# Kernel optimization log

Measured on AMD Instinct MI355X. Metric: run time of the kernel, lower is better.

## Reference

```python
import jax, jax.numpy as jnp
import numpy as np

B, T, I, H = 32768, 200, 6, 6
FF, OUT = 128, 12


def setup_inputs() -> dict:
    key = jax.random.key(0)
    ks = jax.random.split(key, 10)
    s = lambda fan_in: 1.0 / np.sqrt(fan_in)
    inp = {
        "x": jax.random.normal(ks[0], (B, T, I), dtype=jnp.float32),
        # PyTorch LSTM params (gate order i, f, g, o)
        "W_ih": jax.random.uniform(ks[1], (4 * H, I), jnp.float32, -s(H), s(H)),
        "W_hh": jax.random.uniform(ks[2], (4 * H, H), jnp.float32, -s(H), s(H)),
        "b_ih": jax.random.uniform(ks[3], (4 * H,), jnp.float32, -s(H), s(H)),
        "b_hh": jax.random.uniform(ks[4], (4 * H,), jnp.float32, -s(H), s(H)),
        # MLP head (Dropout is identity in eval mode)
        "W1": jax.random.uniform(ks[5], (FF, T * H), jnp.float32, -s(T * H), s(T * H)),
        "b1": jax.random.uniform(ks[6], (FF,), jnp.float32, -s(T * H), s(T * H)),
        "W2": jax.random.uniform(ks[7], (OUT, FF), jnp.float32, -s(FF), s(FF)),
        "b2": jax.random.uniform(ks[8], (OUT,), jnp.float32, -s(FF), s(FF)),
    }
    return inp


def _lstm(x, W_ih, W_hh, b_ih, b_hh):
    # x: [B, T, I] -> hidden sequence [B, T, H]
    # Precompute input projections for all timesteps at once: [T, B, 4H]
    xg = jnp.einsum("bti,gi->tbg", x, W_ih) + (b_ih + b_hh)
    h0 = jnp.zeros((x.shape[0], H), x.dtype)
    c0 = jnp.zeros((x.shape[0], H), x.dtype)

    def step(carry, xg_t):
        h, c = carry
        gates = xg_t + h @ W_hh.T  # [B, 4H]
        i, f, g, o = jnp.split(gates, 4, axis=-1)
        i = jax.nn.sigmoid(i)
        f = jax.nn.sigmoid(f)
        g = jnp.tanh(g)
        o = jax.nn.sigmoid(o)
        c = f * c + i * g
        h = o * jnp.tanh(c)
        return (h, c), h

    _, hs = jax.lax.scan(step, (h0, c0), xg)  # hs: [T, B, H]
    return jnp.transpose(hs, (1, 0, 2))  # [B, T, H]


def reference(x, W_ih, W_hh, b_ih, b_hh, W1, b1, W2, b2):
    hs = _lstm(x, W_ih, W_hh, b_ih, b_hh)          # [B, T, H]
    flat = hs.reshape(hs.shape[0], -1)             # [B, T*H]
    hid = jax.nn.relu(flat @ W1.T + b1)            # [B, 128]
    return hid @ W2.T + b2                         # [B, 12]
```

## Files before the change

### kernel.cpp

```cpp
#include <hip/hip_runtime.h>
#include <hip/hip_bf16.h>

#define Bn   32768
#define Tn   200
#define In   6
#define Hn   6
#define FFn  128
#define OUTn 12
#define KP   1600

typedef __attribute__((ext_vector_type(2))) float          f32x2;
typedef __attribute__((ext_vector_type(4))) float          f32x4;
typedef __attribute__((ext_vector_type(8))) short          bf16x8;
typedef __attribute__((ext_vector_type(4))) unsigned short u16x4;
typedef __attribute__((ext_vector_type(8))) unsigned short u16x8;

#define LOG2E 1.442695041f

__device__ __forceinline__ f32x2 pkfma(f32x2 a, f32x2 b, f32x2 c) {
#if __has_builtin(__builtin_elementwise_fma)
    return __builtin_elementwise_fma(a, b, c);
#else
    return a * b + c;
#endif
}
__device__ __forceinline__ float rcp1p(float e) {
    return __builtin_amdgcn_rcpf(1.f + __builtin_amdgcn_exp2f(e));
}
__device__ __forceinline__ float tanh_c(float c) {
    return fmaf(-2.f, rcp1p(2.f * LOG2E * c), 1.f);
}
__device__ __forceinline__ float swap1(float v) {
    return __int_as_float(__builtin_amdgcn_mov_dpp(__float_as_int(v), 0xB1, 0xF, 0xF, true));
}
__device__ __forceinline__ unsigned short f2bf(float v) {
    unsigned u = __float_as_uint(v);
    unsigned r = u + 0x7FFFu + ((u >> 16) & 1u);
    return (unsigned short)(r >> 16);
}

#define BAR() do {                                          \
    asm volatile("s_waitcnt lgkmcnt(0)" ::: "memory");      \
    __builtin_amdgcn_sched_barrier(0);                      \
    __builtin_amdgcn_s_barrier();                           \
    __builtin_amdgcn_sched_barrier(0);                      \
} while (0)

__global__ void prep_kernel(const float* __restrict__ W1, unsigned short* __restrict__ W1p) {
    int idx = blockIdx.x * 256 + threadIdx.x;
    if (idx >= FFn * KP) return;
    int ff = idx / KP, kp = idx - ff * KP;
    int t = kp >> 3, p = kp & 7;
    float v = 0.f;
    if (p != 3 && p != 7) {
        int h = (p < 3) ? p : (p - 1);
        v = W1[ff * (Tn * Hn) + t * Hn + h];
    }
    W1p[idx] = f2bf(v);
}

__global__ __launch_bounds__(256, 1)
void fused_kernel(const float* __restrict__ x,
                  const float* __restrict__ W_ih, const float* __restrict__ W_hh,
                  const float* __restrict__ b_ih, const float* __restrict__ b_hh,
                  const unsigned short* __restrict__ W1p,
                  const float* __restrict__ b1,
                  const float* __restrict__ W2, const float* __restrict__ b2,
                  float* __restrict__ out)
{
    __shared__ unsigned short htile[2][8][128][8];
    __shared__ unsigned short hidS[128][136];
    __shared__ float          W2s[OUTn * FFn];

    const int tid  = threadIdx.x;
    const int sloc = tid >> 1;
    const int role = tid & 1;
    const int b0   = blockIdx.x * 128;
    const int wv   = tid >> 6;
    const int l    = tid & 63;
    const int lr   = l & 15;
    const int lg   = l >> 4;

    f32x2 Wx[6][6], Wh[6][6], bias2[6];
    #pragma unroll
    for (int gt = 0; gt < 4; ++gt) {
        #pragma unroll
        for (int m = 0; m < 3; ++m) {
            const int j = gt * 3 + m;
            const int p = j >> 1, hf = j & 1;
            const int row = gt * 6 + role * 3 + m;
            const float sc = (gt == 2) ? (2.f * LOG2E) : (-LOG2E);
            #pragma unroll
            for (int k = 0; k < 6; ++k) Wx[p][k][hf] = sc * W_ih[row * 6 + k];
            #pragma unroll
            for (int k = 0; k < 3; ++k) Wh[p][k][hf]     = sc * W_hh[row * 6 + role * 3 + k];
            #pragma unroll
            for (int k = 0; k < 3; ++k) Wh[p][3 + k][hf] = sc * W_hh[row * 6 + (1 - role) * 3 + k];
            bias2[p][hf] = sc * (b_ih[row] + b_hh[row]);
        }
    }

    float hOwn[3] = {0.f, 0.f, 0.f}, hOth[3] = {0.f, 0.f, 0.f}, cS[3] = {0.f, 0.f, 0.f};

    f32x4 acc[8][2];
    #pragma unroll
    for (int m = 0; m < 8; ++m)
        #pragma unroll
        for (int n = 0; n < 2; ++n)
            acc[m][n] = (f32x4){0.f, 0.f, 0.f, 0.f};

    const f32x4* xb4 = (const f32x4*)(x + (size_t)(b0 + sloc) * (Tn * In));

    const unsigned short* wrow[2];
    #pragma unroll
    for (int n = 0; n < 2; ++n) wrow[n] = W1p + (size_t)(wv * 32 + n * 16 + lr) * KP;

    auto LOADB = [&](int g, bf16x8 (&bf)[2][2]) {
        #pragma unroll
        for (int kc = 0; kc < 2; ++kc)
            #pragma unroll
            for (int n = 0; n < 2; ++n)
                bf[kc][n] = *((const bf16x8*)&wrow[n][g * 64 + kc * 32 + lg * 8]);
    };

    auto STEPS8 = [&](const f32x4 (&bx)[12], int slot) {
        #pragma unroll
        for (int s = 0; s < 8; ++s) {
            float xv[6];
            #pragma unroll
            for (int k = 0; k < 6; ++k) { const int fl = s * 6 + k; xv[k] = bx[fl >> 2][fl & 3]; }
            f32x2 a2[6];
            #pragma unroll
            for (int p = 0; p < 6; ++p) a2[p] = bias2[p];
            #pragma unroll
            for (int k = 0; k < 6; ++k) {
                const f32x2 xs = (f32x2){xv[k], xv[k]};
                #pragma unroll
                for (int p = 0; p < 6; ++p) a2[p] = pkfma(Wx[p][k], xs, a2[p]);
            }
            #pragma unroll
            for (int k = 0; k < 3; ++k) {
                const f32x2 hs = (f32x2){hOwn[k], hOwn[k]};
                #pragma unroll
                for (int p = 0; p < 6; ++p) a2[p] = pkfma(Wh[p][k], hs, a2[p]);
            }
            #pragma unroll
            for (int k = 0; k < 3; ++k) {
                const f32x2 hs = (f32x2){hOth[k], hOth[k]};
                #pragma unroll
                for (int p = 0; p < 6; ++p) a2[p] = pkfma(Wh[p][3 + k], hs, a2[p]);
            }
            float av[12];
            #pragma unroll
            for (int p = 0; p < 6; ++p) { av[2 * p] = a2[p][0]; av[2 * p + 1] = a2[p][1]; }

            unsigned short hb[3];
            #pragma unroll
            for (int m = 0; m < 3; ++m) {
                const float iv = rcp1p(av[m]);
                const float fv = rcp1p(av[3 + m]);
                const float gv = fmaf(-2.f, rcp1p(av[6 + m]), 1.f);
                const float ov = rcp1p(av[9 + m]);
                const float c  = fmaf(fv, cS[m], iv * gv);
                cS[m] = c;
                const float hv = ov * tanh_c(c);
                hOwn[m] = hv;
                hOth[m] = swap1(hv);
                hb[m]   = f2bf(hv);
            }
            u16x4 hw; hw.x = hb[0]; hw.y = hb[1]; hw.z = hb[2]; hw.w = 0;
            *((u16x4*)&htile[slot][s][sloc][role * 4]) = hw;
        }
    };

    auto MFMAG8 = [&](int slot, const bf16x8 (&bf)[2][2]) {
        #pragma unroll
        for (int kc = 0; kc < 2; ++kc) {
            bf16x8 af[8];
            #pragma unroll
            for (int m = 0; m < 8; ++m)
                af[m] = *((const bf16x8*)&htile[slot][kc * 4 + lg][m * 16 + lr][0]);
            #pragma unroll
            for (int n = 0; n < 2; ++n)
                #pragma unroll
                for (int m = 0; m < 8; ++m)
                    acc[m][n] = __builtin_amdgcn_mfma_f32_16x16x32_bf16(af[m], bf[kc][n], acc[m][n], 0, 0, 0);
        }
    };

    f32x4 bufA[12], bufB[12];
    #pragma unroll
    for (int q = 0; q < 12; ++q) bufA[q] = xb4[q];
    bf16x8 bfA[2][2], bfB[2][2];

    for (int gg = 0; gg < 12; ++gg) {
        const int gA = 2 * gg, gB = gA + 1;
        #pragma unroll
        for (int q = 0; q < 12; ++q) bufB[q] = xb4[gB * 12 + q];
        LOADB(gA, bfA);
        STEPS8(bufA, 0);
        BAR();
        #pragma unroll
        for (int q = 0; q < 12; ++q) bufA[q] = xb4[(gB + 1) * 12 + q];
        MFMAG8(0, bfA);
        LOADB(gB, bfB);
        STEPS8(bufB, 1);
        BAR();
        MFMAG8(1, bfB);
    }
    LOADB(24, bfA);
    STEPS8(bufA, 0);
    BAR();
    MFMAG8(0, bfA);

    float b1v[2];
    #pragma unroll
    for (int n = 0; n < 2; ++n) b1v[n] = b1[wv * 32 + n * 16 + lr];
    #pragma unroll
    for (int m = 0; m < 8; ++m)
        #pragma unroll
        for (int n = 0; n < 2; ++n)
            #pragma unroll
            for (int r = 0; r < 4; ++r)
                hidS[m * 16 + lg * 4 + r][wv * 32 + n * 16 + lr] =
                    f2bf(fmaxf(acc[m][n][r] + b1v[n], 0.f));
    for (int q = tid; q < OUTn * FFn; q += 256) W2s[q] = W2[q];
    __syncthreads();

    const int s2 = tid >> 1;
    const int half = tid & 1;
    float oa[6];
    #pragma unroll
    for (int jj = 0; jj < 6; ++jj) oa[jj] = b2[half * 6 + jj];
    for (int k8 = 0; k8 < 16; ++k8) {
        const u16x8 hv8 = *((const u16x8*)&hidS[s2][k8 * 8]);
        #pragma unroll
        for (int e = 0; e < 8; ++e) {
            const float hv = __uint_as_float(((unsigned)(unsigned short)hv8[e]) << 16);
            const int k = k8 * 8 + e;
            #pragma unroll
            for (int jj = 0; jj < 6; ++jj)
                oa[jj] = fmaf(hv, W2s[(half * 6 + jj) * FFn + k], oa[jj]);
        }
    }
    float* op = out + (size_t)(b0 + s2) * OUTn + half * 6;
    #pragma unroll
    for (int jj = 0; jj < 6; ++jj) op[jj] = oa[jj];
}

extern "C" void kernel_launch(void* const* d_in, const int* in_sizes, int n_in,
                              void* d_out, int out_size, void* d_ws, size_t ws_size,
                              hipStream_t stream) {
    const float* x    = (const float*)d_in[0];
    const float* W_ih = (const float*)d_in[1];
    const float* W_hh = (const float*)d_in[2];
    const float* b_ih = (const float*)d_in[3];
    const float* b_hh = (const float*)d_in[4];
    const float* W1   = (const float*)d_in[5];
    const float* b1   = (const float*)d_in[6];
    const float* W2   = (const float*)d_in[7];
    const float* b2   = (const float*)d_in[8];
    unsigned short* W1p = (unsigned short*)d_ws;
    float* out = (float*)d_out;

    prep_kernel<<<(FFn * KP + 255) / 256, 256, 0, stream>>>(W1, W1p);
    fused_kernel<<<Bn / 128, 256, 0, stream>>>(x, W_ih, W_hh, b_ih, b_hh,
                                               W1p, b1, W2, b2, out);
}
```

Baseline: 116.4 us.

## Merge LSTM gate reciprocals and restructure x prefetch into half-group buffers

```diff
diff --git a/kernel.cpp b/kernel.cpp
--- a/kernel.cpp
+++ b/kernel.cpp
@@ -23,12 +23,6 @@
 #else
     return a * b + c;
 #endif
-}
-__device__ __forceinline__ float rcp1p(float e) {
-    return __builtin_amdgcn_rcpf(1.f + __builtin_amdgcn_exp2f(e));
-}
-__device__ __forceinline__ float tanh_c(float c) {
-    return fmaf(-2.f, rcp1p(2.f * LOG2E * c), 1.f);
 }
 __device__ __forceinline__ float swap1(float v) {
     return __int_as_float(__builtin_amdgcn_mov_dpp(__float_as_int(v), 0xB1, 0xF, 0xF, true));
@@ -123,9 +117,9 @@
                 bf[kc][n] = *((const bf16x8*)&wrow[n][g * 64 + kc * 32 + lg * 8]);
     };
 
-    auto STEPS8 = [&](const f32x4 (&bx)[12], int slot) {
-        #pragma unroll
-        for (int s = 0; s < 8; ++s) {
+    auto STEPS4 = [&](const f32x4 (&bx)[6], int slot, int sbase) {
+        #pragma unroll
+        for (int s = 0; s < 4; ++s) {
             float xv[6];
             #pragma unroll
             for (int k = 0; k < 6; ++k) { const int fl = s * 6 + k; xv[k] = bx[fl >> 2][fl & 3]; }
@@ -157,19 +151,25 @@
             unsigned short hb[3];
             #pragma unroll
             for (int m = 0; m < 3; ++m) {
-                const float iv = rcp1p(av[m]);
-                const float fv = rcp1p(av[3 + m]);
-                const float gv = fmaf(-2.f, rcp1p(av[6 + m]), 1.f);
-                const float ov = rcp1p(av[9 + m]);
-                const float c  = fmaf(fv, cS[m], iv * gv);
+                const float Ei = __builtin_amdgcn_exp2f(av[m]);
+                const float Ef = __builtin_amdgcn_exp2f(av[3 + m]);
+                const float Eg = __builtin_amdgcn_exp2f(av[6 + m]);
+                const float Eo = __builtin_amdgcn_exp2f(av[9 + m]);
+                const float fv = __builtin_amdgcn_rcpf(1.f + Ef);
+                const float ig = (Eg - 1.f) *
+                                 __builtin_amdgcn_rcpf((1.f + Ei) * (1.f + Eg));
+                float c = fmaf(fv, cS[m], ig);
+                c = fminf(fmaxf(c, -30.f), 30.f);
                 cS[m] = c;
-                const float hv = ov * tanh_c(c);
+                const float Ec = __builtin_amdgcn_exp2f(2.f * LOG2E * c);
+                const float hv = (Ec - 1.f) *
+                                 __builtin_amdgcn_rcpf((1.f + Eo) * (1.f + Ec));
                 hOwn[m] = hv;
                 hOth[m] = swap1(hv);
                 hb[m]   = f2bf(hv);
             }
             u16x4 hw; hw.x = hb[0]; hw.y = hb[1]; hw.z = hb[2]; hw.w = 0;
-            *((u16x4*)&htile[slot][s][sloc][role * 4]) = hw;
+            *((u16x4*)&htile[slot][sbase + s][sloc][role * 4]) = hw;
         }
     };
 
@@ -188,30 +188,24 @@
         }
     };
 
-    f32x4 bufA[12], bufB[12];
-    #pragma unroll
-    for (int q = 0; q < 12; ++q) bufA[q] = xb4[q];
-    bf16x8 bfA[2][2], bfB[2][2];
-
-    for (int gg = 0; gg < 12; ++gg) {
-        const int gA = 2 * gg, gB = gA + 1;
-        #pragma unroll
-        for (int q = 0; q < 12; ++q) bufB[q] = xb4[gB * 12 + q];
-        LOADB(gA, bfA);
-        STEPS8(bufA, 0);
+    f32x4 bufA[6], bufB[6];
+    #pragma unroll
+    for (int q = 0; q < 6; ++q) bufA[q] = xb4[q];
+    bf16x8 bfg[2][2];
+
+    for (int g = 0; g < 25; ++g) {
+        #pragma unroll
+        for (int q = 0; q < 6; ++q) bufB[q] = xb4[(2 * g + 1) * 6 + q];
+        STEPS4(bufA, g & 1, 0);
+        LOADB(g, bfg);
+        if (g < 24) {
+            #pragma unroll
+            for (int q = 0; q < 6; ++q) bufA[q] = xb4[(2 * g + 2) * 6 + q];
+        }
+        STEPS4(bufB, g & 1, 4);
         BAR();
-        #pragma unroll
-        for (int q = 0; q < 12; ++q) bufA[q] = xb4[(gB + 1) * 12 + q];
-        MFMAG8(0, bfA);
-        LOADB(gB, bfB);
-        STEPS8(bufB, 1);
-        BAR();
-        MFMAG8(1, bfB);
-    }
-    LOADB(24, bfA);
-    STEPS8(bufA, 0);
-    BAR();
-    MFMAG8(0, bfA);
+        MFMAG8(g & 1, bfg);
+    }
 
     float b1v[2];
     #pragma unroll
```

After: 123.8 us. 1.06x slower.
